# Kernel tuning notes

Hardware: AMD Instinct MI355X
Metric: run time of the kernel (lower is better)

## Reference

```python
import jax, jax.numpy as jnp
import numpy as np

EPS = 1e-12  # clamp for sqrt stability in Gram-matrix distance

def _pairwise_euclid(X, Y):
    # [B,D],[M,D] -> [B,M] Euclidean distances via Gram trick (avoids [B,M,D] diff tensor)
    x2 = jnp.sum(X * X, axis=-1, keepdims=True)        # [B,1]
    y2 = jnp.sum(Y * Y, axis=-1)[None, :]              # [1,M]
    sq = x2 + y2 - 2.0 * (X @ Y.T)
    return jnp.sqrt(jnp.maximum(sq, EPS))

def setup_inputs() -> dict:
    key = jax.random.key(0)
    k1, k2, k3 = jax.random.split(key, 3)
    B, D = 4096, 128
    return {
        "rep_anchor": jax.random.normal(k1, (B, D), dtype=jnp.float32),
        "rep_pos": jax.random.normal(k2, (B, D), dtype=jnp.float32),
        "rep_neg": jax.random.normal(k3, (B, D), dtype=jnp.float32),
    }

def reference(rep_anchor, rep_pos, rep_neg):
    B = rep_anchor.shape[0]
    # distance_pos[i] = ||a_i - p_i||_2 (elementwise rows, like F.pairwise_distance)
    diff = rep_anchor - rep_pos
    distance_pos = jnp.sqrt(jnp.maximum(jnp.sum(diff * diff, axis=-1), EPS))  # [B]

    big = jnp.asarray(jnp.finfo(rep_anchor.dtype).max, rep_anchor.dtype)
    eye = jnp.eye(B, dtype=bool)
    # anchor-as-negative: exclude self (index i)
    d_aa = jnp.where(eye, big, _pairwise_euclid(rep_anchor, rep_anchor))  # [B,B]
    # pos-as-negative: rep_pos[i] is excluded for anchor i
    d_ap = jnp.where(eye, big, _pairwise_euclid(rep_anchor, rep_pos))    # [B,B]
    # all of rep_neg are negatives
    d_an = _pairwise_euclid(rep_anchor, rep_neg)                          # [B,B]

    hardest_neg = jnp.minimum(jnp.minimum(d_aa.min(axis=1), d_ap.min(axis=1)), d_an.min(axis=1))  # [B]
    # log1p(exp(x)) == softplus, computed stably
    loss_in_batch = jnp.logaddexp(0.0, distance_pos - hardest_neg)
    return jnp.mean(loss_in_batch)
```

## Files before the change

### kernel.cpp

```cpp
#include <hip/hip_runtime.h>
#include <math.h>

#define BDIM 4096
#define DDIM 128
#define EPSF 1e-12f
#define TI 128
#define TJ 64
#define NSPLIT 16
#define NSLICE (NSPLIT * 2)
#define ITILES (BDIM / TI)
#define TILES_PER_MAT (BDIM / TJ)
#define TOTAL_JT (3 * TILES_PER_MAT)
#define JT_PER_SPLIT (TOTAL_JT / NSPLIT)
#define FLT_BIG 3.402823466e+38f
#define MATSZ (BDIM * DDIM)

typedef __attribute__((ext_vector_type(8))) _Float16 f16x8;
typedef __attribute__((ext_vector_type(16))) float f32x16;

__device__ __forceinline__ void gload_lds16(const void* g, void* l) {
    __builtin_amdgcn_global_load_lds(
        (const __attribute__((address_space(1))) unsigned int*)(uintptr_t)g,
        (__attribute__((address_space(3))) unsigned int*)(unsigned int)(uintptr_t)l,
        16, 0, 0);
}

__device__ __forceinline__ unsigned int pack2h(float x, float y) {
    _Float16 hx = (_Float16)x, hy = (_Float16)y;
    unsigned short ux, uy;
    __builtin_memcpy(&ux, &hx, 2);
    __builtin_memcpy(&uy, &hy, 2);
    return (unsigned int)ux | ((unsigned int)uy << 16);
}

__global__ __launch_bounds__(256) void prep_kernel(
    const float* __restrict__ A, const float* __restrict__ P,
    const float* __restrict__ N, ushort* __restrict__ Xf,
    float* __restrict__ a2, float* __restrict__ p2,
    float* __restrict__ n2, float* __restrict__ dpos) {
    int row = (blockIdx.x * blockDim.x + threadIdx.x) >> 6;
    int lane = threadIdx.x & 63;
    if (row >= BDIM) return;
    const float2 av = *(const float2*)&A[row * DDIM + lane * 2];
    const float2 pv = *(const float2*)&P[row * DDIM + lane * 2];
    const float2 nv = *(const float2*)&N[row * DDIM + lane * 2];
    *(unsigned int*)&Xf[0 * MATSZ + row * DDIM + lane * 2] = pack2h(av.x, av.y);
    *(unsigned int*)&Xf[1 * MATSZ + row * DDIM + lane * 2] = pack2h(pv.x, pv.y);
    *(unsigned int*)&Xf[2 * MATSZ + row * DDIM + lane * 2] = pack2h(nv.x, nv.y);
    float sa = av.x * av.x + av.y * av.y;
    float sp = pv.x * pv.x + pv.y * pv.y;
    float sn = nv.x * nv.x + nv.y * nv.y;
    float dx = av.x - pv.x, dy = av.y - pv.y;
    float sd = dx * dx + dy * dy;
    #pragma unroll
    for (int off = 32; off; off >>= 1) {
        sa += __shfl_down(sa, off);
        sp += __shfl_down(sp, off);
        sn += __shfl_down(sn, off);
        sd += __shfl_down(sd, off);
    }
    if (lane == 0) {
        a2[row] = sa;
        p2[row] = sp;
        n2[row] = sn;
        dpos[row] = sqrtf(fmaxf(sd, EPSF));
    }
}

__device__ __forceinline__ void stage_Y(const ushort* g, int j0, ushort* dst,
                                        int w, int lane) {
    int sub = lane >> 4;
    int s = lane & 15;
    #pragma unroll
    for (int q = 0; q < 4; ++q) {
        int r = w * 16 + q * 4 + sub;
        int sp = s ^ (r & 15);
        gload_lds16(g + (size_t)(j0 + r) * DDIM + sp * 8,
                    dst + (w * 16 + q * 4) * DDIM);
    }
}

__global__ __launch_bounds__(256, 2) void minsq_kernel(
    const ushort* __restrict__ Xf,
    const float* __restrict__ a2, const float* __restrict__ p2,
    const float* __restrict__ n2, float* __restrict__ partial) {
    __shared__ __align__(16) ushort Ah[TI * DDIM];
    __shared__ __align__(16) ushort Yh[2][TJ * DDIM];

    const int tid = threadIdx.x;
    const int w = tid >> 6;
    const int lane = tid & 63;
    const int rg = w >> 1;
    const int ch = w & 1;
    const int iTile = blockIdx.x;
    const int split = blockIdx.y;
    const int i0 = iTile * TI;

    {
        int sub = lane >> 4, s = lane & 15;
        #pragma unroll
        for (int q = 0; q < 8; ++q) {
            int r = w * 32 + q * 4 + sub;
            int sp = s ^ (r & 15);
            gload_lds16(Xf + (size_t)(i0 + r) * DDIM + sp * 8,
                        Ah + (w * 32 + q * 4) * DDIM);
        }
    }
    const int jt0 = split * JT_PER_SPLIT;
    stage_Y(Xf + (size_t)(jt0 >> 6) * MATSZ, (jt0 & 63) * TJ, Yh[0], w, lane);
    __syncthreads();

    f16x8 afr[2][8];
    #pragma unroll
    for (int rb = 0; rb < 2; ++rb) {
        int r = rg * 64 + rb * 32 + (lane & 31);
        #pragma unroll
        for (int t = 0; t < 8; ++t) {
            int sl = t * 2 + (lane >> 5);
            int sp = sl ^ (r & 15);
            afr[rb][t] = *(const f16x8*)&Ah[r * DDIM + sp * 8];
        }
    }

    float minv[2][16];
    #pragma unroll
    for (int rb = 0; rb < 2; ++rb)
        #pragma unroll
        for (int g = 0; g < 16; ++g) minv[rb][g] = FLT_BIG;

    for (int idx = 0; idx < JT_PER_SPLIT; ++idx) {
        const int jt = jt0 + idx;
        const int m = jt >> 6;
        const int tc = jt & 63;
        const int cur = idx & 1;

        if (idx + 1 < JT_PER_SPLIT) {
            int jn = jt + 1;
            stage_Y(Xf + (size_t)(jn >> 6) * MATSZ, (jn & 63) * TJ,
                    Yh[cur ^ 1], w, lane);
        }

        f32x16 acc0 = {};
        f32x16 acc1 = {};
        {
            int r = ch * 32 + (lane & 31);
            #pragma unroll
            for (int t = 0; t < 8; ++t) {
                int sl = t * 2 + (lane >> 5);
                int sp = sl ^ (r & 15);
                f16x8 b = *(const f16x8*)&Yh[cur][r * DDIM + sp * 8];
                acc0 = __builtin_amdgcn_mfma_f32_32x32x16_f16(afr[0][t], b, acc0, 0, 0, 0);
                acc1 = __builtin_amdgcn_mfma_f32_32x32x16_f16(afr[1][t], b, acc1, 0, 0, 0);
            }
        }

        const float* y2g = (m == 0) ? a2 : ((m == 1) ? p2 : n2);
        const int jg = tc * TJ + ch * 32 + (lane & 31);
        const float y2h = 0.5f * y2g[jg];
        if (m < 2 && (tc >> 1) == iTile) {
            #pragma unroll
            for (int rb = 0; rb < 2; ++rb) {
                #pragma unroll
                for (int g = 0; g < 16; ++g) {
                    int rloc = (g & 3) + 8 * (g >> 2) + 4 * (lane >> 5);
                    int ig = i0 + rg * 64 + rb * 32 + rloc;
                    float d = (rb == 0) ? acc0[g] : acc1[g];
                    float cand = y2h - d;
                    if (ig == jg) cand = FLT_BIG;
                    minv[rb][g] = fminf(minv[rb][g], cand);
                }
            }
        } else {
            #pragma unroll
            for (int g = 0; g < 16; ++g) {
                minv[0][g] = fminf(minv[0][g], y2h - acc0[g]);
                minv[1][g] = fminf(minv[1][g], y2h - acc1[g]);
            }
        }
        __syncthreads();
    }

    #pragma unroll
    for (int off = 1; off < 32; off <<= 1) {
        #pragma unroll
        for (int rb = 0; rb < 2; ++rb)
            #pragma unroll
            for (int g = 0; g < 16; ++g)
                minv[rb][g] = fminf(minv[rb][g], __shfl_xor(minv[rb][g], off));
    }
    if ((lane & 31) == 0) {
        int hi = lane >> 5;
        #pragma unroll
        for (int rb = 0; rb < 2; ++rb) {
            #pragma unroll
            for (int g = 0; g < 16; ++g) {
                int rloc = (g & 3) + 8 * (g >> 2) + 4 * hi;
                int ig = i0 + rg * 64 + rb * 32 + rloc;
                partial[(split * 2 + ch) * BDIM + ig] = minv[rb][g];
            }
        }
    }
}

__global__ __launch_bounds__(256) void lossA_kernel(
    const float* __restrict__ partial, const float* __restrict__ a2,
    const float* __restrict__ dpos, float* __restrict__ bsum) {
    __shared__ float red[4];
    int i = blockIdx.x * 256 + threadIdx.x;
    float mv = FLT_BIG;
    #pragma unroll
    for (int s = 0; s < NSLICE; ++s) mv = fminf(mv, partial[s * BDIM + i]);
    float h2 = a2[i] + 2.0f * mv;
    float hardest = sqrtf(fmaxf(h2, EPSF));
    float x = dpos[i] - hardest;
    float sum = fmaxf(x, 0.f) + log1pf(expf(-fabsf(x)));
    #pragma unroll
    for (int off = 32; off; off >>= 1) sum += __shfl_down(sum, off);
    if ((threadIdx.x & 63) == 0) red[threadIdx.x >> 6] = sum;
    __syncthreads();
    if (threadIdx.x == 0)
        bsum[blockIdx.x] = red[0] + red[1] + red[2] + red[3];
}

__global__ void lossB_kernel(const float* __restrict__ bsum,
                             float* __restrict__ out) {
    float v = (threadIdx.x < 16) ? bsum[threadIdx.x] : 0.f;
    #pragma unroll
    for (int off = 32; off; off >>= 1) v += __shfl_down(v, off);
    if (threadIdx.x == 0) out[0] = v * (1.0f / BDIM);
}

extern "C" void kernel_launch(void* const* d_in, const int* in_sizes, int n_in,
                              void* d_out, int out_size, void* d_ws, size_t ws_size,
                              hipStream_t stream) {
    const float* A = (const float*)d_in[0];
    const float* P = (const float*)d_in[1];
    const float* N = (const float*)d_in[2];

    float* ws = (float*)d_ws;
    float* a2 = ws;
    float* p2 = ws + BDIM;
    float* n2 = ws + 2 * BDIM;
    float* dpos = ws + 3 * BDIM;
    float* bsum = ws + 4 * BDIM;
    float* partial = ws + 4 * BDIM + 64;
    ushort* Xf = (ushort*)(partial + (size_t)NSLICE * BDIM);

    prep_kernel<<<BDIM / 4, 256, 0, stream>>>(A, P, N, Xf, a2, p2, n2, dpos);
    dim3 grid2(ITILES, NSPLIT);
    minsq_kernel<<<grid2, 256, 0, stream>>>(Xf, a2, p2, n2, partial);
    lossA_kernel<<<16, 256, 0, stream>>>(partial, a2, dpos, bsum);
    lossB_kernel<<<1, 64, 0, stream>>>(bsum, (float*)d_out);
}
```

Before: 35.65 us.

## Use four-slot LDS ring with depth-two prefetch and vmcnt-based waits

Replaces the double-buffered Y staging and separate A buffer with a four-slot LDS pool: A occupies the first two slots and is reused as Y ring slots once its fragments are in registers. Y tiles are prefetched two tiles ahead, and each iteration uses explicit vmcnt waits and a single s_barrier in place of the trailing __syncthreads. The y2 norms are preloaded into registers and MFMA sections get raised priority. The partial-min layout is transposed so the loss kernel reads each row's slices with vectorized float4 loads. The hand-counted vmcnt values and the reuse of the A region as ring slots are fragile if the load counts change.

```diff
diff --git a/kernel.cpp b/kernel.cpp
--- a/kernel.cpp
+++ b/kernel.cpp
@@ -9,11 +9,10 @@
 #define NSPLIT 16
 #define NSLICE (NSPLIT * 2)
 #define ITILES (BDIM / TI)
-#define TILES_PER_MAT (BDIM / TJ)
-#define TOTAL_JT (3 * TILES_PER_MAT)
-#define JT_PER_SPLIT (TOTAL_JT / NSPLIT)
+#define JT 12
 #define FLT_BIG 3.402823466e+38f
 #define MATSZ (BDIM * DDIM)
+#define YBUF (TJ * DDIM)
 
 typedef __attribute__((ext_vector_type(8))) _Float16 f16x8;
 typedef __attribute__((ext_vector_type(16))) float f32x16;
@@ -84,8 +83,8 @@
     const ushort* __restrict__ Xf,
     const float* __restrict__ a2, const float* __restrict__ p2,
     const float* __restrict__ n2, float* __restrict__ partial) {
-    __shared__ __align__(16) ushort Ah[TI * DDIM];
-    __shared__ __align__(16) ushort Yh[2][TJ * DDIM];
+    __shared__ __align__(16) ushort pool[4][YBUF];
+    ushort* const base = &pool[0][0];
 
     const int tid = threadIdx.x;
     const int w = tid >> 6;
@@ -95,20 +94,23 @@
     const int iTile = blockIdx.x;
     const int split = blockIdx.y;
     const int i0 = iTile * TI;
-
-    {
-        int sub = lane >> 4, s = lane & 15;
-        #pragma unroll
-        for (int q = 0; q < 8; ++q) {
-            int r = w * 32 + q * 4 + sub;
-            int sp = s ^ (r & 15);
-            gload_lds16(Xf + (size_t)(i0 + r) * DDIM + sp * 8,
-                        Ah + (w * 32 + q * 4) * DDIM);
-        }
-    }
-    const int jt0 = split * JT_PER_SPLIT;
-    stage_Y(Xf + (size_t)(jt0 >> 6) * MATSZ, (jt0 & 63) * TJ, Yh[0], w, lane);
-    __syncthreads();
+    const int jt0 = split * JT;
+    const int sub = lane >> 4, s = lane & 15;
+
+    #pragma unroll
+    for (int q = 0; q < 8; ++q) {
+        int r = w * 32 + q * 4 + sub;
+        int sp = s ^ (r & 15);
+        gload_lds16(Xf + (size_t)(i0 + r) * DDIM + sp * 8,
+                    base + (w * 32 + q * 4) * DDIM);
+    }
+    stage_Y(Xf + (size_t)(jt0 >> 6) * MATSZ, (jt0 & 63) * TJ, base + 2 * YBUF, w, lane);
+    stage_Y(Xf + (size_t)((jt0 + 1) >> 6) * MATSZ, ((jt0 + 1) & 63) * TJ,
+            base + 3 * YBUF, w, lane);
+
+    asm volatile("s_waitcnt vmcnt(8)" ::: "memory");
+    __builtin_amdgcn_s_barrier();
+    __builtin_amdgcn_sched_barrier(0);
 
     f16x8 afr[2][8];
     #pragma unroll
@@ -118,9 +120,20 @@
         for (int t = 0; t < 8; ++t) {
             int sl = t * 2 + (lane >> 5);
             int sp = sl ^ (r & 15);
-            afr[rb][t] = *(const f16x8*)&Ah[r * DDIM + sp * 8];
-        }
-    }
+            afr[rb][t] = *(const f16x8*)&base[r * DDIM + sp * 8];
+        }
+    }
+    float y2h[JT];
+    #pragma unroll
+    for (int t = 0; t < JT; ++t) {
+        int jt = jt0 + t, m = jt >> 6, tc = jt & 63;
+        const float* y2g = (m == 0) ? a2 : ((m == 1) ? p2 : n2);
+        y2h[t] = 0.5f * y2g[tc * TJ + ch * 32 + (lane & 31)];
+    }
+    asm volatile("s_waitcnt lgkmcnt(0)" ::: "memory");
+    __builtin_amdgcn_sched_barrier(0);
+    __builtin_amdgcn_s_barrier();
+    __builtin_amdgcn_sched_barrier(0);
 
     float minv[2][16];
     #pragma unroll
@@ -128,56 +141,61 @@
         #pragma unroll
         for (int g = 0; g < 16; ++g) minv[rb][g] = FLT_BIG;
 
-    for (int idx = 0; idx < JT_PER_SPLIT; ++idx) {
-        const int jt = jt0 + idx;
-        const int m = jt >> 6;
-        const int tc = jt & 63;
-        const int cur = idx & 1;
-
-        if (idx + 1 < JT_PER_SPLIT) {
-            int jn = jt + 1;
+    #pragma unroll
+    for (int idx = 0; idx < JT; ++idx) {
+        if (idx + 2 < JT) {
+            int jn = jt0 + idx + 2;
             stage_Y(Xf + (size_t)(jn >> 6) * MATSZ, (jn & 63) * TJ,
-                    Yh[cur ^ 1], w, lane);
-        }
-
+                    base + (idx & 3) * YBUF, w, lane);
+        }
+        if (idx < JT - 2)       asm volatile("s_waitcnt vmcnt(8)" ::: "memory");
+        else if (idx == JT - 2) asm volatile("s_waitcnt vmcnt(4)" ::: "memory");
+        else                    asm volatile("s_waitcnt vmcnt(0)" ::: "memory");
+        __builtin_amdgcn_s_barrier();
+        __builtin_amdgcn_sched_barrier(0);
+
+        const ushort* bufY = base + ((idx + 2) & 3) * YBUF;
         f32x16 acc0 = {};
         f32x16 acc1 = {};
         {
             int r = ch * 32 + (lane & 31);
+            __builtin_amdgcn_s_setprio(1);
             #pragma unroll
             for (int t = 0; t < 8; ++t) {
                 int sl = t * 2 + (lane >> 5);
                 int sp = sl ^ (r & 15);
-                f16x8 b = *(const f16x8*)&Yh[cur][r * DDIM + sp * 8];
+                f16x8 b = *(const f16x8*)&bufY[r * DDIM + sp * 8];
                 acc0 = __builtin_amdgcn_mfma_f32_32x32x16_f16(afr[0][t], b, acc0, 0, 0, 0);
                 acc1 = __builtin_amdgcn_mfma_f32_32x32x16_f16(afr[1][t], b, acc1, 0, 0, 0);
             }
-        }
-
-        const float* y2g = (m == 0) ? a2 : ((m == 1) ? p2 : n2);
-        const int jg = tc * TJ + ch * 32 + (lane & 31);
-        const float y2h = 0.5f * y2g[jg];
-        if (m < 2 && (tc >> 1) == iTile) {
-            #pragma unroll
-            for (int rb = 0; rb < 2; ++rb) {
+            __builtin_amdgcn_s_setprio(0);
+        }
+
+        {
+            int jt = jt0 + idx, m = jt >> 6, tc = jt & 63;
+            float yh = y2h[idx];
+            if (m < 2 && (tc >> 1) == iTile) {
+                int jg = tc * TJ + ch * 32 + (lane & 31);
+                #pragma unroll
+                for (int rb = 0; rb < 2; ++rb) {
+                    #pragma unroll
+                    for (int g = 0; g < 16; ++g) {
+                        int rloc = (g & 3) + 8 * (g >> 2) + 4 * (lane >> 5);
+                        int ig = i0 + rg * 64 + rb * 32 + rloc;
+                        float d = (rb == 0) ? acc0[g] : acc1[g];
+                        float cand = yh - d;
+                        if (ig == jg) cand = FLT_BIG;
+                        minv[rb][g] = fminf(minv[rb][g], cand);
+                    }
+                }
+            } else {
                 #pragma unroll
                 for (int g = 0; g < 16; ++g) {
-                    int rloc = (g & 3) + 8 * (g >> 2) + 4 * (lane >> 5);
-                    int ig = i0 + rg * 64 + rb * 32 + rloc;
-                    float d = (rb == 0) ? acc0[g] : acc1[g];
-                    float cand = y2h - d;
-                    if (ig == jg) cand = FLT_BIG;
-                    minv[rb][g] = fminf(minv[rb][g], cand);
+                    minv[0][g] = fminf(minv[0][g], yh - acc0[g]);
+                    minv[1][g] = fminf(minv[1][g], yh - acc1[g]);
                 }
             }
-        } else {
-            #pragma unroll
-            for (int g = 0; g < 16; ++g) {
-                minv[0][g] = fminf(minv[0][g], y2h - acc0[g]);
-                minv[1][g] = fminf(minv[1][g], y2h - acc1[g]);
-            }
-        }
-        __syncthreads();
+        }
     }
 
     #pragma unroll
@@ -190,13 +208,14 @@
     }
     if ((lane & 31) == 0) {
         int hi = lane >> 5;
+        int slice = split * 2 + ch;
         #pragma unroll
         for (int rb = 0; rb < 2; ++rb) {
             #pragma unroll
             for (int g = 0; g < 16; ++g) {
                 int rloc = (g & 3) + 8 * (g >> 2) + 4 * hi;
                 int ig = i0 + rg * 64 + rb * 32 + rloc;
-                partial[(split * 2 + ch) * BDIM + ig] = minv[rb][g];
+                partial[(size_t)ig * NSLICE + slice] = minv[rb][g];
             }
         }
     }
@@ -207,9 +226,13 @@
     const float* __restrict__ dpos, float* __restrict__ bsum) {
     __shared__ float red[4];
     int i = blockIdx.x * 256 + threadIdx.x;
+    const float4* pr = (const float4*)&partial[(size_t)i * NSLICE];
     float mv = FLT_BIG;
     #pragma unroll
-    for (int s = 0; s < NSLICE; ++s) mv = fminf(mv, partial[s * BDIM + i]);
+    for (int q = 0; q < NSLICE / 4; ++q) {
+        float4 v = pr[q];
+        mv = fminf(mv, fminf(fminf(v.x, v.y), fminf(v.z, v.w)));
+    }
     float h2 = a2[i] + 2.0f * mv;
     float hardest = sqrtf(fmaxf(h2, EPSF));
     float x = dpos[i] - hardest;
```

New measurement: 35.58 us. Within noise of the previous version (-0.2%).
